# Kernel tuning notes

Hardware: AMD Instinct MI355X
Metric: run time of the kernel (lower is better)

The kernel has to match this reference:

```python
import jax, jax.numpy as jnp
import numpy as np

# --- model dims (from init_kwargs: d_model=2048, num_heads=16, d_conv=4, expand_v=2) ---
D_MODEL = 2048
N_HEADS = 16
D_HEAD = D_MODEL // N_HEADS          # 128
EXPAND_V = 2
KEY_DIM = N_HEADS * D_HEAD           # 2048
VALUE_DIM = KEY_DIM * EXPAND_V       # 4096
HEAD_V = D_HEAD * EXPAND_V           # 256
D_CONV = 4
CONV_CH = 2 * KEY_DIM + VALUE_DIM    # 8192 (q,k,v channels)
TOTAL_PROJ = 2 * KEY_DIM + 2 * VALUE_DIM + 2 * N_HEADS  # 12320
SPLITS = np.cumsum([KEY_DIM, KEY_DIM, VALUE_DIM, VALUE_DIM, N_HEADS]).tolist()


def setup_inputs() -> dict:
    key = jax.random.key(0)
    k0, k1, k2, k3 = jax.random.split(key, 4)
    B, L = 2, 2048
    return {
        "hidden_states": jax.random.normal(k0, (B, L, D_MODEL), jnp.float32),
        "W_qkvgba": jax.random.normal(k1, (D_MODEL, TOTAL_PROJ), jnp.float32) * 0.02,
        "W_conv": jax.random.normal(k2, (CONV_CH, D_CONV), jnp.float32) * 0.1,
        "A_log": jax.random.normal(k3, (N_HEADS,), jnp.float32) * 0.1,
        "dt_bias": jnp.zeros((N_HEADS,), jnp.float32),
    }


def _l2norm(x, eps=1e-6):
    return x * jax.lax.rsqrt(jnp.sum(x * x, axis=-1, keepdims=True) + eps)


def reference(hidden_states, W_qkvgba, W_conv, A_log, dt_bias):
    B, L, _ = hidden_states.shape
    # fused qkv / gate / beta / A projection
    proj = hidden_states @ W_qkvgba                      # [B, L, 12320]
    q, k, v, gate, b, A = jnp.split(proj, SPLITS, axis=-1)

    # depthwise causal short conv over q,k,v channels, then SiLU
    qkv = jnp.concatenate([q, k, v], axis=-1)            # [B, L, CONV_CH]
    x = qkv.transpose(0, 2, 1)                           # [B, C, L]
    kern = W_conv[:, None, :]                            # [C, 1, D_CONV]
    y = jax.lax.conv_general_dilated(
        x, kern, window_strides=(1,), padding=[(D_CONV - 1, 0)],
        feature_group_count=CONV_CH)
    y = jax.nn.silu(y).transpose(0, 2, 1)                # [B, L, C]
    q, k, v = jnp.split(y, [KEY_DIM, 2 * KEY_DIM], axis=-1)

    q = q.reshape(B, L, N_HEADS, D_HEAD)
    k = k.reshape(B, L, N_HEADS, D_HEAD)
    v = v.reshape(B, L, N_HEADS, HEAD_V)

    # L2 norm of q,k (use_qk_l2norm_in_kernel=True)
    q = _l2norm(q)
    k = _l2norm(k)
    scale = D_HEAD ** -0.5

    beta = jax.nn.sigmoid(b)                             # [B, L, H]
    g = -jnp.exp(A_log) * jax.nn.softplus(A + dt_bias)   # [B, L, H] (log decay <= 0)

    # gated delta-rule recurrence over time (scan); state S: [B, H, dk, dv]
    qT = q.transpose(1, 0, 2, 3)
    kT = k.transpose(1, 0, 2, 3)
    vT = v.transpose(1, 0, 2, 3)
    gT = g.transpose(1, 0, 2)
    bT = beta.transpose(1, 0, 2)

    def step(S, inp):
        qt, kt, vt, gt, bt = inp
        S = S * jnp.exp(gt)[..., None, None]
        kv = jnp.einsum('bhk,bhkv->bhv', kt, S)          # current memory readout at k
        delta = (vt - kv) * bt[..., None]                # delta-rule error, gated by beta
        S = S + jnp.einsum('bhk,bhv->bhkv', kt, delta)
        ot = jnp.einsum('bhk,bhkv->bhv', qt * scale, S)
        return S, ot

    S0 = jnp.zeros((B, N_HEADS, D_HEAD, HEAD_V), jnp.float32)
    _, oT = jax.lax.scan(step, S0, (qT, kT, vT, gT, bT))
    o = oT.transpose(1, 0, 2, 3)                         # [B, L, H, HEAD_V]

    # output gating: o * silu(gate)
    gate = gate.reshape(B, L, N_HEADS, HEAD_V)
    return o * jax.nn.silu(gate)
```

## Files before the change

### kernel.cpp

```cpp
#include <hip/hip_runtime.h>
#include <hip/hip_bf16.h>
#include <hip/hip_fp16.h>
#include <math.h>

#define L_SEQ 2048
#define DM    2048
#define NH    16
#define DH    128
#define HVD   256
#define NPROJ 12320
#define QKVW  8192
#define GW    4128

#define NTILE_N 97
#define KSTEPS  64

typedef _Float16 v8h __attribute__((ext_vector_type(8)));
typedef float f32x4 __attribute__((ext_vector_type(4)));
typedef float f32x16 __attribute__((ext_vector_type(16)));

__device__ __forceinline__ void gload_lds16(const void* g, void* l) {
  __builtin_amdgcn_global_load_lds((const __attribute__((address_space(1))) void*)g,
                                   (__attribute__((address_space(3))) void*)l, 16, 0, 0);
}

__device__ __forceinline__ void splitw(float x, unsigned short& h, unsigned short& l) {
  _Float16 hh = (_Float16)x;
  _Float16 ll = (_Float16)(x - (float)hh);
  h = *(unsigned short*)&hh;
  l = *(unsigned short*)&ll;
}
__device__ __forceinline__ float h2f(unsigned short u) {
  return (float)(*(_Float16*)&u);
}

#define MFMA3(acc, ah, al, bh_, bl_)                                          \
  acc = __builtin_amdgcn_mfma_f32_16x16x32_f16(ah, bh_, acc, 0, 0, 0);        \
  acc = __builtin_amdgcn_mfma_f32_16x16x32_f16(ah, bl_, acc, 0, 0, 0);        \
  acc = __builtin_amdgcn_mfma_f32_16x16x32_f16(al, bh_, acc, 0, 0, 0);

#define MFMA3W(acc, ah, al, bh_, bl_)                                         \
  acc = __builtin_amdgcn_mfma_f32_32x32x16_f16(ah, bh_, acc, 0, 0, 0);        \
  acc = __builtin_amdgcn_mfma_f32_32x32x16_f16(ah, bl_, acc, 0, 0, 0);        \
  acc = __builtin_amdgcn_mfma_f32_32x32x16_f16(al, bh_, acc, 0, 0, 0);

__global__ __launch_bounds__(256) void pack_A_k(const float* __restrict__ H, _Float16* __restrict__ Ap) {
  const int mtile = blockIdx.x >> 6, kstep = blockIdx.x & 63;
  const size_t base = (size_t)blockIdx.x * 2 * 4096;
#pragma unroll
  for (int it = 0; it < 2; ++it) {
    int s = threadIdx.x + it * 256;
    int g = s >> 7, r = s & 127;
    const float* src = H + ((size_t)(mtile * 128 + r)) * 2048 + kstep * 32 + g * 8;
    float4 x0 = *(const float4*)src;
    float4 x1 = *(const float4*)(src + 4);
    float xs[8] = {x0.x, x0.y, x0.z, x0.w, x1.x, x1.y, x1.z, x1.w};
    v8h hi, lo;
#pragma unroll
    for (int j = 0; j < 8; ++j) {
      float v = xs[j] * 16.f;
      _Float16 h = (_Float16)v;
      hi[j] = h;
      lo[j] = (_Float16)(v - (float)h);
    }
    *(v8h*)(Ap + base + g * 1024 + r * 8) = hi;
    *(v8h*)(Ap + base + 4096 + g * 1024 + r * 8) = lo;
  }
}

__global__ __launch_bounds__(256) void pack_B_k(const float* __restrict__ W, _Float16* __restrict__ Bp) {
  const int ntile = blockIdx.x >> 6, kstep = blockIdx.x & 63;
  const size_t base = (size_t)blockIdx.x * 2 * 4096;
#pragma unroll
  for (int it = 0; it < 2; ++it) {
    int s = threadIdx.x + it * 256;
    int g = s >> 7, col = s & 127;
    int n = ntile * 128 + col;
    v8h hi, lo;
#pragma unroll
    for (int j = 0; j < 8; ++j) {
      int k = kstep * 32 + g * 8 + j;
      float v = (n < NPROJ) ? W[(size_t)k * NPROJ + n] * 1024.f : 0.f;
      _Float16 h = (_Float16)v;
      hi[j] = h;
      lo[j] = (_Float16)(v - (float)h);
    }
    *(v8h*)(Bp + base + g * 1024 + col * 8) = hi;
    *(v8h*)(Bp + base + 4096 + g * 1024 + col * 8) = lo;
  }
}

__global__ __launch_bounds__(256) void gemm_mfma_k(const _Float16* __restrict__ Ap,
                                                   const _Float16* __restrict__ Bp,
                                                   float* __restrict__ Cq,
                                                   float* __restrict__ Cg) {
  __shared__ _Float16 lds[2][16384];
  const int tid = threadIdx.x;
  const int mtile = blockIdx.x & 31;
  const int ntile = blockIdx.x >> 5;
  const int wid = tid >> 6, lane = tid & 63;
  const int wm = wid >> 1, wn = wid & 1;
  const int lrow = lane & 31, kg = lane >> 5;

  f32x16 acc[2][2];
#pragma unroll
  for (int i = 0; i < 2; ++i)
#pragma unroll
    for (int j = 0; j < 2; ++j)
#pragma unroll
      for (int r = 0; r < 16; ++r) acc[i][j][r] = 0.f;

  const int arow0 = (wm * 64 + lrow) * 8;
  const int bcol0 = (wn * 64 + lrow) * 8;

  const _Float16* Asrc = Ap + ((size_t)(mtile * KSTEPS) * 2) * 4096 + tid * 8;
  const _Float16* Bsrc = Bp + ((size_t)(ntile * KSTEPS) * 2) * 4096 + tid * 8;

#define STAGE(KS, BUF)                                                         \
  {                                                                            \
    const _Float16* An_ = Asrc + (size_t)(KS) * 8192;                          \
    const _Float16* Bn_ = Bsrc + (size_t)(KS) * 8192;                          \
    _Pragma("unroll")                                                          \
    for (int r = 0; r < 4; ++r) {                                              \
      gload_lds16(An_ + r * 2048, &lds[BUF][r * 2048 + tid * 8]);              \
      gload_lds16(Bn_ + r * 2048, &lds[BUF][8192 + r * 2048 + tid * 8]);       \
    }                                                                          \
  }

  STAGE(0, 0);
  STAGE(1, 1);

  for (int kstep = 0; kstep < KSTEPS; ++kstep) {
    const int p = kstep & 1;
    if (kstep + 1 < KSTEPS) {
      asm volatile("s_waitcnt vmcnt(8)" ::: "memory");
    } else {
      asm volatile("s_waitcnt vmcnt(0)" ::: "memory");
    }
    __builtin_amdgcn_sched_barrier(0);
    __builtin_amdgcn_s_barrier();
    __builtin_amdgcn_sched_barrier(0);

#pragma unroll
    for (int ksub = 0; ksub < 2; ++ksub) {
      const int base = (ksub * 2 + kg) * 1024;
      v8h ah0 = *(const v8h*)&lds[p][base + arow0];
      v8h ah1 = *(const v8h*)&lds[p][base + arow0 + 256];
      v8h al0 = *(const v8h*)&lds[p][4096 + base + arow0];
      v8h al1 = *(const v8h*)&lds[p][4096 + base + arow0 + 256];
      v8h bh0 = *(const v8h*)&lds[p][8192 + base + bcol0];
      v8h bh1 = *(const v8h*)&lds[p][8192 + base + bcol0 + 256];
      v8h bl0 = *(const v8h*)&lds[p][12288 + base + bcol0];
      v8h bl1 = *(const v8h*)&lds[p][12288 + base + bcol0 + 256];
      MFMA3W(acc[0][0], ah0, al0, bh0, bl0);
      MFMA3W(acc[0][1], ah0, al0, bh1, bl1);
      MFMA3W(acc[1][0], ah1, al1, bh0, bl0);
      MFMA3W(acc[1][1], ah1, al1, bh1, bl1);
    }
    __builtin_amdgcn_sched_barrier(0);
    __builtin_amdgcn_s_barrier();
    __builtin_amdgcn_sched_barrier(0);
    if (kstep + 2 < KSTEPS) STAGE(kstep + 2, p);
  }
#undef STAGE

  const float sc = 1.f / 16384.f;
#pragma unroll
  for (int tm = 0; tm < 2; ++tm)
#pragma unroll
    for (int tn = 0; tn < 2; ++tn) {
      int col = ntile * 128 + wn * 64 + tn * 32 + lrow;
#pragma unroll
      for (int r = 0; r < 16; ++r) {
        int row = mtile * 128 + wm * 64 + tm * 32 + (r & 3) + 8 * (r >> 2) + 4 * kg;
        float v = acc[tm][tn][r] * sc;
        if (col < QKVW) {
          Cq[(size_t)row * QKVW + col] = v;
        } else if (col < NPROJ) {
          Cg[(size_t)row * GW + (col - QKVW)] = v;
        }
      }
    }
}

__global__ __launch_bounds__(64) void conv_qk_k(
    const float* __restrict__ projQKV, const float* __restrict__ Wc,
    float* __restrict__ qn, float* __restrict__ kn)
{
  const int b = blockIdx.z, hg = blockIdx.y, tc = blockIdx.x;
  const int lane = threadIdx.x;
  const int ch = hg * 128 + lane * 2;
  float4 Wa = *(const float4*)(Wc + (size_t)ch * 4);
  float4 Wb = *(const float4*)(Wc + (size_t)ch * 4 + 4);
  const int t0 = tc * 64;
  const float* P = projQKV + (size_t)b * L_SEQ * QKVW + ch;
  float2 w0 = make_float2(0.f, 0.f), w1 = w0, w2 = w0;
  if (t0 >= 3) w0 = *(const float2*)(P + (size_t)(t0 - 3) * QKVW);
  if (t0 >= 2) w1 = *(const float2*)(P + (size_t)(t0 - 2) * QKVW);
  if (t0 >= 1) w2 = *(const float2*)(P + (size_t)(t0 - 1) * QKVW);
  const bool isq = hg < 16;
  const int h = isq ? hg : hg - 16;
  float* dst = (isq ? qn : kn) + (((size_t)b * NH + h) * L_SEQ) * DH + lane * 2;
  const float sc = isq ? 0.08838834764831845f : 1.f;
  for (int t = t0; t < t0 + 64; ++t) {
    float2 x = *(const float2*)(P + (size_t)t * QKVW);
    float y0 = w0.x * Wa.x + w1.x * Wa.y + w2.x * Wa.z + x.x * Wa.w;
    float y1 = w0.y * Wb.x + w1.y * Wb.y + w2.y * Wb.z + x.y * Wb.w;
    w0 = w1; w1 = w2; w2 = x;
    y0 = y0 / (1.f + expf(-y0));
    y1 = y1 / (1.f + expf(-y1));
    float ss = y0 * y0 + y1 * y1;
#pragma unroll
    for (int off = 1; off < 64; off <<= 1) ss += __shfl_xor(ss, off);
    float nrm = sc / sqrtf(ss + 1e-6f);
    *(float2*)(dst + (size_t)t * DH) = make_float2(y0 * nrm, y1 * nrm);
  }
}

__global__ __launch_bounds__(256) void conv_v_k(
    const float* __restrict__ projQKV, const float* __restrict__ Wc,
    float* __restrict__ vn)
{
  const int b = blockIdx.z, cg = blockIdx.y, tc = blockIdx.x;
  const int vc = (cg * 256 + threadIdx.x) * 4;
  const int ch = 4096 + vc;
  float4 Wv0 = *(const float4*)(Wc + (size_t)ch * 4);
  float4 Wv1 = *(const float4*)(Wc + (size_t)ch * 4 + 4);
  float4 Wv2 = *(const float4*)(Wc + (size_t)ch * 4 + 8);
  float4 Wv3 = *(const float4*)(Wc + (size_t)ch * 4 + 12);
  const int t0 = tc * 64;
  const float* P = projQKV + (size_t)b * L_SEQ * QKVW + ch;
  float4 w0 = make_float4(0.f, 0.f, 0.f, 0.f), w1 = w0, w2 = w0;
  if (t0 >= 3) w0 = *(const float4*)(P + (size_t)(t0 - 3) * QKVW);
  if (t0 >= 2) w1 = *(const float4*)(P + (size_t)(t0 - 2) * QKVW);
  if (t0 >= 1) w2 = *(const float4*)(P + (size_t)(t0 - 1) * QKVW);
  const int h = vc >> 8, vcol = vc & 255;
  float* dst = vn + (((size_t)b * NH + h) * L_SEQ) * HVD + vcol;
  for (int t = t0; t < t0 + 64; ++t) {
    float4 x = *(const float4*)(P + (size_t)t * QKVW);
    float4 y;
    y.x = w0.x * Wv0.x + w1.x * Wv0.y + w2.x * Wv0.z + x.x * Wv0.w;
    y.y = w0.y * Wv1.x + w1.y * Wv1.y + w2.y * Wv1.z + x.y * Wv1.w;
    y.z = w0.z * Wv2.x + w1.z * Wv2.y + w2.z * Wv2.z + x.z * Wv2.w;
    y.w = w0.w * Wv3.x + w1.w * Wv3.y + w2.w * Wv3.z + x.w * Wv3.w;
    w0 = w1; w1 = w2; w2 = x;
    y.x = y.x / (1.f + expf(-y.x));
    y.y = y.y / (1.f + expf(-y.y));
    y.z = y.z / (1.f + expf(-y.z));
    y.w = y.w / (1.f + expf(-y.w));
    *(float4*)(dst + (size_t)t * HVD) = y;
  }
}

__global__ __launch_bounds__(256) void beta_g_k(
    const float* __restrict__ projGate, const float* __restrict__ A_log,
    const float* __restrict__ dt_bias, float* __restrict__ beta, float* __restrict__ g_out)
{
  int idx = blockIdx.x * 256 + threadIdx.x;
  if (idx >= 2 * NH * L_SEQ) return;
  int t = idx & (L_SEQ - 1);
  int h = (idx >> 11) & (NH - 1);
  int b = idx >> 15;
  size_t row = (size_t)(b * L_SEQ + t) * GW;
  float bv = projGate[row + 4096 + h];
  float av = projGate[row + 4112 + h];
  float be = 1.f / (1.f + expf(-bv));
  float xx = av + dt_bias[h];
  float sp = (xx > 20.f) ? xx : log1pf(expf(xx));
  float g = -expf(A_log[h]) * sp;
  beta[idx] = be;
  g_out[idx] = g;
}

__global__ __launch_bounds__(256) void p1_k(
    const float* __restrict__ kn, const float* __restrict__ qn,
    const float* __restrict__ g_arr, const float* __restrict__ beta_arr,
    _Float16* __restrict__ Tg_h, _Float16* __restrict__ Tg_l,
    _Float16* __restrict__ Hg_h, _Float16* __restrict__ Hg_l,
    _Float16* __restrict__ KTg_h, _Float16* __restrict__ KTg_l,
    float* __restrict__ coefG)
{
  __shared__ _Float16 Kh[8192], Kl[8192];
  __shared__ _Float16 QS[16384];
  __shared__ float lc[64], be[64], kw[64];
  _Float16* Qh = QS;
  _Float16* Ql = QS + 8192;
  float* Am = (float*)QS;
  float* Tm = Am + 4096;
  const int cid = blockIdx.x, bh = cid >> 5, ch = cid & 31, t0 = ch * 64;
  const int tid = threadIdx.x, w = tid >> 6, lane = tid & 63, lr = lane & 15, g16 = lane >> 4;

  const float* kb = kn + ((size_t)bh * 2048 + t0) * 128;
  const float* qb = qn + ((size_t)bh * 2048 + t0) * 128;
#pragma unroll
  for (int l = 0; l < 8; ++l) {
    int s = tid + l * 256;
    int row = s >> 5, c = (s & 31) * 4;
    int ad = row * 128 + (c ^ ((row & 7) << 3));
    float4 v = *(const float4*)(kb + (size_t)row * 128 + c);
    ushort4 H, L;
    splitw(v.x * 1024.f, H.x, L.x); splitw(v.y * 1024.f, H.y, L.y);
    splitw(v.z * 1024.f, H.z, L.z); splitw(v.w * 1024.f, H.w, L.w);
    *(ushort4*)&Kh[ad] = H; *(ushort4*)&Kl[ad] = L;
    float4 q = *(const float4*)(qb + (size_t)row * 128 + c);
    splitw(q.x * 1024.f, H.x, L.x); splitw(q.y * 1024.f, H.y, L.y);
    splitw(q.z * 1024.f, H.z, L.z); splitw(q.w * 1024.f, H.w, L.w);
    *(ushort4*)&Qh[ad] = H; *(ushort4*)&Ql[ad] = L;
  }
  if (tid < 64) {
    float x = g_arr[(size_t)bh * 2048 + t0 + tid];
#pragma unroll
    for (int off = 1; off < 64; off <<= 1) { float y = __shfl_up(x, off); if (tid >= off) x += y; }
    lc[tid] = x;
    float x63 = __shfl(x, 63);
    float b_ = beta_arr[(size_t)bh * 2048 + t0 + tid];
    be[tid] = b_;
    kw[tid] = expf(x63 - x);
    float ca = expf(x);
    coefG[(size_t)cid * 192 + tid] = ca;
    coefG[(size_t)cid * 192 + 64 + tid] = b_;
    coefG[(size_t)cid * 192 + 128 + tid] = b_ * ca;
  }
  __syncthreads();
  const float ds20 = 1.f / 1048576.f;
  const int arow = w * 16 + lr, swa = (arow & 7) << 3;
  f32x4 gacc[4];
  for (int nt = 0; nt < 4; ++nt) {
    f32x4 acc = (f32x4){0.f, 0.f, 0.f, 0.f};
    int nrow = nt * 16 + lr, swn = (nrow & 7) << 3;
#pragma unroll
    for (int ks = 0; ks < 4; ++ks) {
      int c = ks * 32 + g16 * 8;
      v8h ah = *(const v8h*)&Kh[arow * 128 + (c ^ swa)];
      v8h al = *(const v8h*)&Kl[arow * 128 + (c ^ swa)];
      v8h bhh = *(const v8h*)&Kh[nrow * 128 + (c ^ swn)];
      v8h bll = *(const v8h*)&Kl[nrow * 128 + (c ^ swn)];
      MFMA3(acc, ah, al, bhh, bll);
    }
    gacc[nt] = acc;
  }
  for (int nt = 0; nt < 4; ++nt) {
    f32x4 acc = (f32x4){0.f, 0.f, 0.f, 0.f};
    int nrow = nt * 16 + lr, swn = (nrow & 7) << 3;
#pragma unroll
    for (int ks = 0; ks < 4; ++ks) {
      int c = ks * 32 + g16 * 8;
      v8h ah = *(const v8h*)&Qh[arow * 128 + (c ^ swa)];
      v8h al = *(const v8h*)&Ql[arow * 128 + (c ^ swa)];
      v8h bhh = *(const v8h*)&Kh[nrow * 128 + (c ^ swn)];
      v8h bll = *(const v8h*)&Kl[nrow * 128 + (c ^ swn)];
      MFMA3(acc, ah, al, bhh, bll);
    }
    int s_ = nt * 16 + lr;
#pragma unroll
    for (int r = 0; r < 4; ++r) {
      int t = w * 16 + g16 * 4 + r;
      float hv = (s_ <= t) ? acc[r] * ds20 * expf(lc[t] - lc[s_]) : 0.f;
      unsigned short hh, ll; splitw(hv * 16384.f, hh, ll);
      size_t go = (size_t)cid * 4096 + t * 64 + (s_ ^ ((t & 7) << 3));
      *(unsigned short*)&Hg_h[go] = hh;
      *(unsigned short*)&Hg_l[go] = ll;
    }
  }
  __syncthreads();
  for (int nt = 0; nt < 4; ++nt) {
    int s_ = nt * 16 + lr;
#pragma unroll
    for (int r = 0; r < 4; ++r) {
      int t = w * 16 + g16 * 4 + r;
      float av = (s_ < t) ? gacc[nt][r] * ds20 * be[t] * expf(lc[t] - lc[s_]) : 0.f;
      Am[t * 64 + s_] = av;
    }
  }
#pragma unroll
  for (int l = 0; l < 16; ++l) { int s2 = tid + l * 256; Tm[s2] = ((s2 >> 6) == (s2 & 63)) ? 1.f : 0.f; }
  for (int s = tid; s < 8192; s += 256) {
    int feat = s >> 6, t = s & 63;
    int ki = t * 128 + (feat ^ ((t & 7) << 3));
    float kvv = ((float)Kh[ki] + (float)Kl[ki]) * kw[t];
    unsigned short hh, ll; splitw(kvv, hh, ll);
    size_t go = (size_t)cid * 8192 + feat * 64 + (t ^ ((feat & 7) << 3));
    *(unsigned short*)&KTg_h[go] = hh;
    *(unsigned short*)&KTg_l[go] = ll;
  }
  __syncthreads();
  if (w == 0) {
    int j = lane;
    for (int t = 1; t < 64; ++t) {
      float sum = 0.f;
      for (int s = 0; s < t; ++s) sum = fmaf(Am[t * 64 + s], Tm[s * 64 + j], sum);
      Tm[t * 64 + j] = ((j == t) ? 1.f : 0.f) - sum;
    }
  }
  __syncthreads();
#pragma unroll
  for (int l = 0; l < 16; ++l) {
    int s2 = tid + l * 256;
    int t = s2 >> 6, sc_ = s2 & 63;
    unsigned short hh, ll; splitw(Tm[s2] * 256.f, hh, ll);
    size_t go = (size_t)cid * 4096 + t * 64 + (sc_ ^ ((t & 7) << 3));
    *(unsigned short*)&Tg_h[go] = hh;
    *(unsigned short*)&Tg_l[go] = ll;
  }
}

__global__ __launch_bounds__(256) void p2_k(
    const float* __restrict__ qn, const float* __restrict__ kn, const float* __restrict__ vn,
    const float* __restrict__ projGate,
    const _Float16* __restrict__ Tg_h, const _Float16* __restrict__ Tg_l,
    const _Float16* __restrict__ Hg_h, const _Float16* __restrict__ Hg_l,
    const _Float16* __restrict__ KTg_h, const _Float16* __restrict__ KTg_l,
    const float* __restrict__ coefG, float* __restrict__ out)
{
  __shared__ _Float16 St_h[4096], St_l[4096];
  __shared__ _Float16 KQ0[8192], KQ1[8192];
  __shared__ _Float16 KTs_h[8192], KTs_l[8192];
  __shared__ _Float16 Ts_h[4096], Ts_l[4096];
  __shared__ _Float16 Hs_h[4096], Hs_l[4096];
  __shared__ float cf[192];

  const int blk = blockIdx.x;
  const int vb = blk >> 5, bh = blk & 31;
  const int b = bh >> 4, h = bh & 15, v0 = vb * 32;
  const int tid = threadIdx.x, w = tid >> 6, lane = tid & 63, lr = lane & 15, g16 = lane >> 4;

  _Float16* BT_h = &KQ0[0];
  _Float16* BT_l = &KQ0[4096];
  _Float16* UT_h = &KQ1[0];
  _Float16* UT_l = &KQ1[4096];

#pragma unroll
  for (int l = 0; l < 8; ++l) { ((unsigned int*)St_h)[tid + l * 256] = 0u; }
#pragma unroll
  for (int l = 0; l < 8; ++l) { ((unsigned int*)St_l)[tid + l * 256] = 0u; }

  const float* qbase = qn + ((size_t)bh * 2048) * 128;
  const float* kbase = kn + ((size_t)bh * 2048) * 128;
  const float* gp = projGate + ((size_t)b * 2048) * GW + h * 256 + v0;
  const float i2_16 = 1.f / 65536.f;
  const float i2_20 = 1.f / 1048576.f;
  const float uscale = 1.f / 256.f;
  const float sscale = 64.f / 65536.f;

  for (int ch = 0; ch < 32; ++ch) {
    const int cid = bh * 32 + ch, t0 = ch * 64;
    {
      const _Float16* th = Tg_h + (size_t)cid * 4096;
      const _Float16* tl = Tg_l + (size_t)cid * 4096;
      const _Float16* hh = Hg_h + (size_t)cid * 4096;
      const _Float16* hl = Hg_l + (size_t)cid * 4096;
      const _Float16* kth = KTg_h + (size_t)cid * 8192;
      const _Float16* ktl = KTg_l + (size_t)cid * 8192;
#pragma unroll
      for (int l = 0; l < 2; ++l) {
        int i = tid + l * 256;
        gload_lds16(th + i * 8, &Ts_h[i * 8]);
        gload_lds16(tl + i * 8, &Ts_l[i * 8]);
        gload_lds16(hh + i * 8, &Hs_h[i * 8]);
        gload_lds16(hl + i * 8, &Hs_l[i * 8]);
      }
#pragma unroll
      for (int l = 0; l < 4; ++l) {
        int i = tid + l * 256;
        gload_lds16(kth + i * 8, &KTs_h[i * 8]);
        gload_lds16(ktl + i * 8, &KTs_l[i * 8]);
      }
      if (tid < 48) gload_lds16(coefG + (size_t)cid * 192 + tid * 4, &cf[tid * 4]);
#pragma unroll
      for (int l = 0; l < 8; ++l) {
        int s = tid + l * 256;
        int row = s >> 5, c = (s & 31) * 4;
        float4 v = *(const float4*)(qbase + (size_t)(t0 + row) * 128 + c);
        ushort4 H, L;
        splitw(v.x * 1024.f, H.x, L.x); splitw(v.y * 1024.f, H.y, L.y);
        splitw(v.z * 1024.f, H.z, L.z); splitw(v.w * 1024.f, H.w, L.w);
        int ad = row * 128 + (c ^ ((row & 7) << 3));
        *(ushort4*)&KQ0[ad] = H; *(ushort4*)&KQ1[ad] = L;
      }
    }
    __syncthreads();
    const float cc = cf[63];
    f32x4 Oacc[2];
    {
      const int arow = w * 16 + lr, swa = (arow & 7) << 3;
      for (int nt = 0; nt < 2; ++nt) {
        f32x4 acc = (f32x4){0.f, 0.f, 0.f, 0.f};
        const int n = nt * 16 + lr, swn = (n & 7) << 3;
#pragma unroll
        for (int ks = 0; ks < 4; ++ks) {
          int c = ks * 32 + g16 * 8;
          v8h ah = *(const v8h*)&KQ0[arow * 128 + (c ^ swa)];
          v8h al = *(const v8h*)&KQ1[arow * 128 + (c ^ swa)];
          v8h bhh = *(const v8h*)&St_h[n * 128 + (c ^ swn)];
          v8h bll = *(const v8h*)&St_l[n * 128 + (c ^ swn)];
          MFMA3(acc, ah, al, bhh, bll);
        }
        Oacc[nt] = acc;
      }
      float4 cav = *(float4*)&cf[w * 16 + g16 * 4];
#pragma unroll
      for (int nt = 0; nt < 2; ++nt) {
        Oacc[nt][0] *= cav.x * 16.f; Oacc[nt][1] *= cav.y * 16.f;
        Oacc[nt][2] *= cav.z * 16.f; Oacc[nt][3] *= cav.w * 16.f;
      }
    }
    __syncthreads();
#pragma unroll
    for (int l = 0; l < 8; ++l) {
      int s = tid + l * 256;
      int row = s >> 5, c = (s & 31) * 4;
      float4 v = *(const float4*)(kbase + (size_t)(t0 + row) * 128 + c);
      ushort4 H, L;
      splitw(v.x * 1024.f, H.x, L.x); splitw(v.y * 1024.f, H.y, L.y);
      splitw(v.z * 1024.f, H.z, L.z); splitw(v.w * 1024.f, H.w, L.w);
      int ad = row * 128 + (c ^ ((row & 7) << 3));
      *(ushort4*)&KQ0[ad] = H; *(ushort4*)&KQ1[ad] = L;
    }
    __syncthreads();
    ushort4 pBh[2], pBl[2];
    {
      const int arow = w * 16 + lr, swa = (arow & 7) << 3;
      float4 cb1v = *(float4*)&cf[64 + w * 16 + g16 * 4];
      float4 cb2v = *(float4*)&cf[128 + w * 16 + g16 * 4];
      for (int nt = 0; nt < 2; ++nt) {
        f32x4 acc = (f32x4){0.f, 0.f, 0.f, 0.f};
        const int n = nt * 16 + lr, swn = (n & 7) << 3;
#pragma unroll
        for (int ks = 0; ks < 4; ++ks) {
          int c = ks * 32 + g16 * 8;
          v8h ah = *(const v8h*)&KQ0[arow * 128 + (c ^ swa)];
          v8h al = *(const v8h*)&KQ1[arow * 128 + (c ^ swa)];
          v8h bhh = *(const v8h*)&St_h[n * 128 + (c ^ swn)];
          v8h bll = *(const v8h*)&St_l[n * 128 + (c ^ swn)];
          MFMA3(acc, ah, al, bhh, bll);
        }
        float cb1a[4] = {cb1v.x, cb1v.y, cb1v.z, cb1v.w};
        float cb2a[4] = {cb2v.x, cb2v.y, cb2v.z, cb2v.w};
        unsigned short* ph = (unsigned short*)&pBh[nt];
        unsigned short* pl = (unsigned short*)&pBl[nt];
#pragma unroll
        for (int r = 0; r < 4; ++r) {
          int t = w * 16 + g16 * 4 + r;
          float kv = acc[r] * i2_16;
          float Vv = vn[((size_t)bh * 2048 + t0 + t) * 256 + v0 + n];
          float Bv = cb1a[r] * Vv - cb2a[r] * kv;
          splitw(Bv * 64.f, ph[r], pl[r]);
        }
      }
    }
    __syncthreads();
    {
      const int tb = w * 16 + g16 * 4;
      for (int nt = 0; nt < 2; ++nt) {
        const int n = nt * 16 + lr, swn = (n & 7) << 3;
        int ad = n * 64 + (tb ^ swn);
        *(ushort4*)&BT_h[ad] = pBh[nt];
        *(ushort4*)&BT_l[ad] = pBl[nt];
      }
    }
    __syncthreads();
    {
      const int arow = w * 16 + lr, swa = (arow & 7) << 3;
      const int tb = w * 16 + g16 * 4;
      for (int nt = 0; nt < 2; ++nt) {
        f32x4 acc = (f32x4){0.f, 0.f, 0.f, 0.f};
        const int n = nt * 16 + lr, swn = (n & 7) << 3;
#pragma unroll
        for (int ks = 0; ks < 2; ++ks) {
          int c = ks * 32 + g16 * 8;
          v8h ah = *(const v8h*)&Ts_h[arow * 64 + (c ^ swa)];
          v8h al = *(const v8h*)&Ts_l[arow * 64 + (c ^ swa)];
          v8h bhh = *(const v8h*)&BT_h[n * 64 + (c ^ swn)];
          v8h bll = *(const v8h*)&BT_l[n * 64 + (c ^ swn)];
          MFMA3(acc, ah, al, bhh, bll);
        }
        ushort4 H, L;
        unsigned short* ph = (unsigned short*)&H;
        unsigned short* pl = (unsigned short*)&L;
#pragma unroll
        for (int r = 0; r < 4; ++r) splitw(acc[r] * uscale, ph[r], pl[r]);
        int ad = n * 64 + (tb ^ swn);
        *(ushort4*)&UT_h[ad] = H;
        *(ushort4*)&UT_l[ad] = L;
      }
    }
    __syncthreads();
    {
      const int arow = w * 16 + lr, swa = (arow & 7) << 3;
      for (int nt = 0; nt < 2; ++nt) {
        const int n = nt * 16 + lr, swn = (n & 7) << 3;
#pragma unroll
        for (int ks = 0; ks < 2; ++ks) {
          int c = ks * 32 + g16 * 8;
          v8h ah = *(const v8h*)&Hs_h[arow * 64 + (c ^ swa)];
          v8h al = *(const v8h*)&Hs_l[arow * 64 + (c ^ swa)];
          v8h bhh = *(const v8h*)&UT_h[n * 64 + (c ^ swn)];
          v8h bll = *(const v8h*)&UT_l[n * 64 + (c ^ swn)];
          MFMA3(Oacc[nt], ah, al, bhh, bll);
        }
      }
      for (int nt = 0; nt < 2; ++nt) {
        const int n = nt * 16 + lr;
#pragma unroll
        for (int r = 0; r < 4; ++r) {
          int t = t0 + w * 16 + g16 * 4 + r;
          float Ov = Oacc[nt][r] * i2_20;
          float gv = gp[(size_t)t * GW + n];
          out[((size_t)b * 2048 + t) * 4096 + h * 256 + v0 + n] = Ov * (gv / (1.f + expf(-gv)));
        }
      }
    }
    {
      const float cc1024 = cc * 1024.f;
#pragma unroll
      for (int m2 = w * 2; m2 < w * 2 + 2; ++m2) {
        const int arow = m2 * 16 + lr, swa = (arow & 7) << 3;
        const int fb = m2 * 16 + g16 * 4;
        for (int nt = 0; nt < 2; ++nt) {
          const int n = nt * 16 + lr, swn = (n & 7) << 3;
          int sad = n * 128 + (fb ^ swn);
          ushort4 sh4 = *(ushort4*)&St_h[sad];
          ushort4 sl4 = *(ushort4*)&St_l[sad];
          f32x4 acc;
          acc[0] = cc1024 * (h2f(sh4.x) + h2f(sl4.x));
          acc[1] = cc1024 * (h2f(sh4.y) + h2f(sl4.y));
          acc[2] = cc1024 * (h2f(sh4.z) + h2f(sl4.z));
          acc[3] = cc1024 * (h2f(sh4.w) + h2f(sl4.w));
#pragma unroll
          for (int ks = 0; ks < 2; ++ks) {
            int c = ks * 32 + g16 * 8;
            v8h ah = *(const v8h*)&KTs_h[arow * 64 + (c ^ swa)];
            v8h al = *(const v8h*)&KTs_l[arow * 64 + (c ^ swa)];
            v8h bhh = *(const v8h*)&UT_h[n * 64 + (c ^ swn)];
            v8h bll = *(const v8h*)&UT_l[n * 64 + (c ^ swn)];
            MFMA3(acc, ah, al, bhh, bll);
          }
          ushort4 H, L;
          unsigned short* ph = (unsigned short*)&H;
          unsigned short* pl = (unsigned short*)&L;
#pragma unroll
          for (int r = 0; r < 4; ++r) splitw(acc[r] * sscale, ph[r], pl[r]);
          *(ushort4*)&St_h[sad] = H;
          *(ushort4*)&St_l[sad] = L;
        }
      }
    }
    __syncthreads();
  }
}

extern "C" void kernel_launch(void* const* d_in, const int* in_sizes, int n_in,
                              void* d_out, int out_size, void* d_ws, size_t ws_size,
                              hipStream_t stream) {
  const float* hidden  = (const float*)d_in[0];
  const float* W       = (const float*)d_in[1];
  const float* Wc      = (const float*)d_in[2];
  const float* A_log   = (const float*)d_in[3];
  const float* dt_bias = (const float*)d_in[4];
  float* out = (float*)d_out;

  char* ws = (char*)d_ws;
  _Float16* Ap = (_Float16*)ws;
  _Float16* Bp = (_Float16*)(ws + (size_t)33554432);
  float* qn    = (float*)ws;
  float* kn    = qn + (size_t)8388608;
  float* vn    = kn + (size_t)8388608;
  float* g_arr = vn + (size_t)16777216;
  float* beta  = g_arr + (size_t)65536;
  float* projQKV = (float*)(ws + (size_t)135266304);
  char*  tb0 = ws + (size_t)135266304;
  _Float16* Tg_h  = (_Float16*)tb0;
  _Float16* Tg_l  = (_Float16*)(tb0 + (size_t)8388608);
  _Float16* Hg_h  = (_Float16*)(tb0 + (size_t)16777216);
  _Float16* Hg_l  = (_Float16*)(tb0 + (size_t)25165824);
  _Float16* KTg_h = (_Float16*)(tb0 + (size_t)33554432);
  _Float16* KTg_l = (_Float16*)(tb0 + (size_t)50331648);
  float*    coefG = (float*)   (tb0 + (size_t)67108864);
  float* projGate = (float*)(ws + (size_t)269484032);

  pack_A_k<<<32 * KSTEPS, 256, 0, stream>>>(hidden, Ap);
  pack_B_k<<<NTILE_N * KSTEPS, 256, 0, stream>>>(W, Bp);
  gemm_mfma_k<<<32 * NTILE_N, 256, 0, stream>>>(Ap, Bp, projQKV, projGate);

  conv_qk_k<<<dim3(32, 32, 2), 64, 0, stream>>>(projQKV, Wc, qn, kn);
  conv_v_k<<<dim3(32, 4, 2), 256, 0, stream>>>(projQKV, Wc, vn);
  beta_g_k<<<(2 * NH * L_SEQ + 255) / 256, 256, 0, stream>>>(projGate, A_log, dt_bias, beta, g_arr);

  p1_k<<<1024, 256, 0, stream>>>(kn, qn, g_arr, beta, Tg_h, Tg_l, Hg_h, Hg_l, KTg_h, KTg_l, coefG);
  p2_k<<<256, 256, 0, stream>>>(qn, kn, vn, projGate, Tg_h, Tg_l, Hg_h, Hg_l, KTg_h, KTg_l, coefG, out);
}
```

Measured before the change: 1.091 ms.

## Pre-split q/k to swizzled fp16 hi/lo in conv, stream into LDS directly

```diff
diff --git a/kernel.cpp b/kernel.cpp
--- a/kernel.cpp
+++ b/kernel.cpp
@@ -17,7 +17,6 @@
 
 typedef _Float16 v8h __attribute__((ext_vector_type(8)));
 typedef float f32x4 __attribute__((ext_vector_type(4)));
-typedef float f32x16 __attribute__((ext_vector_type(16)));
 
 __device__ __forceinline__ void gload_lds16(const void* g, void* l) {
   __builtin_amdgcn_global_load_lds((const __attribute__((address_space(1))) void*)g,
@@ -38,11 +37,6 @@
   acc = __builtin_amdgcn_mfma_f32_16x16x32_f16(ah, bh_, acc, 0, 0, 0);        \
   acc = __builtin_amdgcn_mfma_f32_16x16x32_f16(ah, bl_, acc, 0, 0, 0);        \
   acc = __builtin_amdgcn_mfma_f32_16x16x32_f16(al, bh_, acc, 0, 0, 0);
-
-#define MFMA3W(acc, ah, al, bh_, bl_)                                         \
-  acc = __builtin_amdgcn_mfma_f32_32x32x16_f16(ah, bh_, acc, 0, 0, 0);        \
-  acc = __builtin_amdgcn_mfma_f32_32x32x16_f16(ah, bl_, acc, 0, 0, 0);        \
-  acc = __builtin_amdgcn_mfma_f32_32x32x16_f16(al, bh_, acc, 0, 0, 0);
 
 __global__ __launch_bounds__(256) void pack_A_k(const float* __restrict__ H, _Float16* __restrict__ Ap) {
   const int mtile = blockIdx.x >> 6, kstep = blockIdx.x & 63;
@@ -100,18 +94,16 @@
   const int ntile = blockIdx.x >> 5;
   const int wid = tid >> 6, lane = tid & 63;
   const int wm = wid >> 1, wn = wid & 1;
-  const int lrow = lane & 31, kg = lane >> 5;
-
-  f32x16 acc[2][2];
-#pragma unroll
-  for (int i = 0; i < 2; ++i)
-#pragma unroll
-    for (int j = 0; j < 2; ++j)
-#pragma unroll
-      for (int r = 0; r < 16; ++r) acc[i][j][r] = 0.f;
-
-  const int arow0 = (wm * 64 + lrow) * 8;
-  const int bcol0 = (wn * 64 + lrow) * 8;
+  const int lrow = lane & 15, g = lane >> 4;
+
+  f32x4 acc[4][4];
+#pragma unroll
+  for (int i = 0; i < 4; ++i)
+#pragma unroll
+    for (int j = 0; j < 4; ++j) acc[i][j] = (f32x4){0.f, 0.f, 0.f, 0.f};
+
+  const int aoff = (wm * 64 + lrow) * 8 + g * 1024;
+  const int boff = (wn * 64 + lrow) * 8 + g * 1024;
 
   const _Float16* Asrc = Ap + ((size_t)(mtile * KSTEPS) * 2) * 4096 + tid * 8;
   const _Float16* Bsrc = Bp + ((size_t)(ntile * KSTEPS) * 2) * 4096 + tid * 8;
@@ -141,22 +133,22 @@
     __builtin_amdgcn_s_barrier();
     __builtin_amdgcn_sched_barrier(0);
 
-#pragma unroll
-    for (int ksub = 0; ksub < 2; ++ksub) {
-      const int base = (ksub * 2 + kg) * 1024;
-      v8h ah0 = *(const v8h*)&lds[p][base + arow0];
-      v8h ah1 = *(const v8h*)&lds[p][base + arow0 + 256];
-      v8h al0 = *(const v8h*)&lds[p][4096 + base + arow0];
-      v8h al1 = *(const v8h*)&lds[p][4096 + base + arow0 + 256];
-      v8h bh0 = *(const v8h*)&lds[p][8192 + base + bcol0];
-      v8h bh1 = *(const v8h*)&lds[p][8192 + base + bcol0 + 256];
-      v8h bl0 = *(const v8h*)&lds[p][12288 + base + bcol0];
-      v8h bl1 = *(const v8h*)&lds[p][12288 + base + bcol0 + 256];
-      MFMA3W(acc[0][0], ah0, al0, bh0, bl0);
-      MFMA3W(acc[0][1], ah0, al0, bh1, bl1);
-      MFMA3W(acc[1][0], ah1, al1, bh0, bl0);
-      MFMA3W(acc[1][1], ah1, al1, bh1, bl1);
-    }
+    v8h ah[4], al[4], bh[4], bl[4];
+#pragma unroll
+    for (int f = 0; f < 4; ++f) {
+      ah[f] = *(const v8h*)&lds[p][aoff + f * 128];
+      al[f] = *(const v8h*)&lds[p][4096 + aoff + f * 128];
+      bh[f] = *(const v8h*)&lds[p][8192 + boff + f * 128];
+      bl[f] = *(const v8h*)&lds[p][12288 + boff + f * 128];
+    }
+#pragma unroll
+    for (int fm = 0; fm < 4; ++fm)
+#pragma unroll
+      for (int fn = 0; fn < 4; ++fn) {
+        acc[fm][fn] = __builtin_amdgcn_mfma_f32_16x16x32_f16(ah[fm], bh[fn], acc[fm][fn], 0, 0, 0);
+        acc[fm][fn] = __builtin_amdgcn_mfma_f32_16x16x32_f16(ah[fm], bl[fn], acc[fm][fn], 0, 0, 0);
+        acc[fm][fn] = __builtin_amdgcn_mfma_f32_16x16x32_f16(al[fm], bh[fn], acc[fm][fn], 0, 0, 0);
+      }
     __builtin_amdgcn_sched_barrier(0);
     __builtin_amdgcn_s_barrier();
     __builtin_amdgcn_sched_barrier(0);
@@ -166,26 +158,29 @@
 
   const float sc = 1.f / 16384.f;
 #pragma unroll
-  for (int tm = 0; tm < 2; ++tm)
-#pragma unroll
-    for (int tn = 0; tn < 2; ++tn) {
-      int col = ntile * 128 + wn * 64 + tn * 32 + lrow;
-#pragma unroll
-      for (int r = 0; r < 16; ++r) {
-        int row = mtile * 128 + wm * 64 + tm * 32 + (r & 3) + 8 * (r >> 2) + 4 * kg;
-        float v = acc[tm][tn][r] * sc;
-        if (col < QKVW) {
-          Cq[(size_t)row * QKVW + col] = v;
-        } else if (col < NPROJ) {
-          Cg[(size_t)row * GW + (col - QKVW)] = v;
-        }
-      }
-    }
+  for (int fm = 0; fm < 4; ++fm) {
+    int row = mtile * 128 + wm * 64 + fm * 16 + g * 4;
+#pragma unroll
+    for (int fn = 0; fn < 4; ++fn) {
+      int col = ntile * 128 + wn * 64 + fn * 16 + lrow;
+      if (col < QKVW) {
+#pragma unroll
+        for (int r = 0; r < 4; ++r)
+          Cq[(size_t)(row + r) * QKVW + col] = acc[fm][fn][r] * sc;
+      } else if (col < NPROJ) {
+        int lcol = col - QKVW;
+#pragma unroll
+        for (int r = 0; r < 4; ++r)
+          Cg[(size_t)(row + r) * GW + lcol] = acc[fm][fn][r] * sc;
+      }
+    }
+  }
 }
 
 __global__ __launch_bounds__(64) void conv_qk_k(
     const float* __restrict__ projQKV, const float* __restrict__ Wc,
-    float* __restrict__ qn, float* __restrict__ kn)
+    _Float16* __restrict__ qh, _Float16* __restrict__ ql,
+    _Float16* __restrict__ kh, _Float16* __restrict__ kl)
 {
   const int b = blockIdx.z, hg = blockIdx.y, tc = blockIdx.x;
   const int lane = threadIdx.x;
@@ -200,8 +195,9 @@
   if (t0 >= 1) w2 = *(const float2*)(P + (size_t)(t0 - 1) * QKVW);
   const bool isq = hg < 16;
   const int h = isq ? hg : hg - 16;
-  float* dst = (isq ? qn : kn) + (((size_t)b * NH + h) * L_SEQ) * DH + lane * 2;
-  const float sc = isq ? 0.08838834764831845f : 1.f;
+  _Float16* dh = (isq ? qh : kh) + (((size_t)b * NH + h) * L_SEQ) * 128;
+  _Float16* dl = (isq ? ql : kl) + (((size_t)b * NH + h) * L_SEQ) * 128;
+  const float sc = (isq ? 0.08838834764831845f : 1.f) * 1024.f;
   for (int t = t0; t < t0 + 64; ++t) {
     float2 x = *(const float2*)(P + (size_t)t * QKVW);
     float y0 = w0.x * Wa.x + w1.x * Wa.y + w2.x * Wa.z + x.x * Wa.w;
@@ -213,7 +209,12 @@
 #pragma unroll
     for (int off = 1; off < 64; off <<= 1) ss += __shfl_xor(ss, off);
     float nrm = sc / sqrtf(ss + 1e-6f);
-    *(float2*)(dst + (size_t)t * DH) = make_float2(y0 * nrm, y1 * nrm);
+    unsigned short h0, l0, h1, l1;
+    splitw(y0 * nrm, h0, l0);
+    splitw(y1 * nrm, h1, l1);
+    int idx = t * 128 + ((lane * 2) ^ ((t & 7) << 3));
+    *(unsigned int*)&dh[idx] = (unsigned int)h0 | ((unsigned int)h1 << 16);
+    *(unsigned int*)&dl[idx] = (unsigned int)l0 | ((unsigned int)l1 << 16);
   }
 }
 
@@ -273,7 +274,8 @@
 }
 
 __global__ __launch_bounds__(256) void p1_k(
-    const float* __restrict__ kn, const float* __restrict__ qn,
+    const _Float16* __restrict__ kh_g, const _Float16* __restrict__ kl_g,
+    const _Float16* __restrict__ qh_g, const _Float16* __restrict__ ql_g,
     const float* __restrict__ g_arr, const float* __restrict__ beta_arr,
     _Float16* __restrict__ Tg_h, _Float16* __restrict__ Tg_l,
     _Float16* __restrict__ Hg_h, _Float16* __restrict__ Hg_l,
@@ -290,22 +292,14 @@
   const int cid = blockIdx.x, bh = cid >> 5, ch = cid & 31, t0 = ch * 64;
   const int tid = threadIdx.x, w = tid >> 6, lane = tid & 63, lr = lane & 15, g16 = lane >> 4;
 
-  const float* kb = kn + ((size_t)bh * 2048 + t0) * 128;
-  const float* qb = qn + ((size_t)bh * 2048 + t0) * 128;
-#pragma unroll
-  for (int l = 0; l < 8; ++l) {
-    int s = tid + l * 256;
-    int row = s >> 5, c = (s & 31) * 4;
-    int ad = row * 128 + (c ^ ((row & 7) << 3));
-    float4 v = *(const float4*)(kb + (size_t)row * 128 + c);
-    ushort4 H, L;
-    splitw(v.x * 1024.f, H.x, L.x); splitw(v.y * 1024.f, H.y, L.y);
-    splitw(v.z * 1024.f, H.z, L.z); splitw(v.w * 1024.f, H.w, L.w);
-    *(ushort4*)&Kh[ad] = H; *(ushort4*)&Kl[ad] = L;
-    float4 q = *(const float4*)(qb + (size_t)row * 128 + c);
-    splitw(q.x * 1024.f, H.x, L.x); splitw(q.y * 1024.f, H.y, L.y);
-    splitw(q.z * 1024.f, H.z, L.z); splitw(q.w * 1024.f, H.w, L.w);
-    *(ushort4*)&Qh[ad] = H; *(ushort4*)&Ql[ad] = L;
+  const size_t gb = ((size_t)bh * 2048 + t0) * 128;
+#pragma unroll
+  for (int l = 0; l < 4; ++l) {
+    int i = (tid + l * 256) * 8;
+    gload_lds16(kh_g + gb + i, &Kh[i]);
+    gload_lds16(kl_g + gb + i, &Kl[i]);
+    gload_lds16(qh_g + gb + i, &Qh[i]);
+    gload_lds16(ql_g + gb + i, &Ql[i]);
   }
   if (tid < 64) {
     float x = g_arr[(size_t)bh * 2048 + t0 + tid];
@@ -405,8 +399,9 @@
 }
 
 __global__ __launch_bounds__(256) void p2_k(
-    const float* __restrict__ qn, const float* __restrict__ kn, const float* __restrict__ vn,
-    const float* __restrict__ projGate,
+    const _Float16* __restrict__ qh_g, const _Float16* __restrict__ ql_g,
+    const _Float16* __restrict__ kh_g, const _Float16* __restrict__ kl_g,
+    const float* __restrict__ vn, const float* __restrict__ projGate,
     const _Float16* __restrict__ Tg_h, const _Float16* __restrict__ Tg_l,
     const _Float16* __restrict__ Hg_h, const _Float16* __restrict__ Hg_l,
     const _Float16* __restrict__ KTg_h, const _Float16* __restrict__ KTg_l,
@@ -414,6 +409,7 @@
 {
   __shared__ _Float16 St_h[4096], St_l[4096];
   __shared__ _Float16 KQ0[8192], KQ1[8192];
+  __shared__ _Float16 KK0[8192], KK1[8192];
   __shared__ _Float16 KTs_h[8192], KTs_l[8192];
   __shared__ _Float16 Ts_h[4096], Ts_l[4096];
   __shared__ _Float16 Hs_h[4096], Hs_l[4096];
@@ -434,8 +430,6 @@
 #pragma unroll
   for (int l = 0; l < 8; ++l) { ((unsigned int*)St_l)[tid + l * 256] = 0u; }
 
-  const float* qbase = qn + ((size_t)bh * 2048) * 128;
-  const float* kbase = kn + ((size_t)bh * 2048) * 128;
   const float* gp = projGate + ((size_t)b * 2048) * GW + h * 256 + v0;
   const float i2_16 = 1.f / 65536.f;
   const float i2_20 = 1.f / 1048576.f;
@@ -451,38 +445,38 @@
       const _Float16* hl = Hg_l + (size_t)cid * 4096;
       const _Float16* kth = KTg_h + (size_t)cid * 8192;
       const _Float16* ktl = KTg_l + (size_t)cid * 8192;
+      const size_t gb = ((size_t)bh * 2048 + t0) * 128;
 #pragma unroll
       for (int l = 0; l < 2; ++l) {
-        int i = tid + l * 256;
-        gload_lds16(th + i * 8, &Ts_h[i * 8]);
-        gload_lds16(tl + i * 8, &Ts_l[i * 8]);
-        gload_lds16(hh + i * 8, &Hs_h[i * 8]);
-        gload_lds16(hl + i * 8, &Hs_l[i * 8]);
+        int i = (tid + l * 256) * 8;
+        gload_lds16(th + i, &Ts_h[i]);
+        gload_lds16(tl + i, &Ts_l[i]);
+        gload_lds16(hh + i, &Hs_h[i]);
+        gload_lds16(hl + i, &Hs_l[i]);
       }
 #pragma unroll
       for (int l = 0; l < 4; ++l) {
-        int i = tid + l * 256;
-        gload_lds16(kth + i * 8, &KTs_h[i * 8]);
-        gload_lds16(ktl + i * 8, &KTs_l[i * 8]);
+        int i = (tid + l * 256) * 8;
+        gload_lds16(kth + i, &KTs_h[i]);
+        gload_lds16(ktl + i, &KTs_l[i]);
+        gload_lds16(qh_g + gb + i, &KQ0[i]);
+        gload_lds16(ql_g + gb + i, &KQ1[i]);
+        gload_lds16(kh_g + gb + i, &KK0[i]);
+        gload_lds16(kl_g + gb + i, &KK1[i]);
       }
       if (tid < 48) gload_lds16(coefG + (size_t)cid * 192 + tid * 4, &cf[tid * 4]);
-#pragma unroll
-      for (int l = 0; l < 8; ++l) {
-        int s = tid + l * 256;
-        int row = s >> 5, c = (s & 31) * 4;
-        float4 v = *(const float4*)(qbase + (size_t)(t0 + row) * 128 + c);
-        ushort4 H, L;
-        splitw(v.x * 1024.f, H.x, L.x); splitw(v.y * 1024.f, H.y, L.y);
-        splitw(v.z * 1024.f, H.z, L.z); splitw(v.w * 1024.f, H.w, L.w);
-        int ad = row * 128 + (c ^ ((row & 7) << 3));
-        *(ushort4*)&KQ0[ad] = H; *(ushort4*)&KQ1[ad] = L;
-      }
-    }
+    }
+    float Vv[2][4];
+#pragma unroll
+    for (int nt = 0; nt < 2; ++nt)
+#pragma unroll
+      for (int r = 0; r < 4; ++r)
+        Vv[nt][r] = vn[((size_t)bh * 2048 + t0 + w * 16 + g16 * 4 + r) * 256 + v0 + nt * 16 + lr];
     __syncthreads();
     const float cc = cf[63];
+    const int arow = w * 16 + lr, swa = (arow & 7) << 3;
     f32x4 Oacc[2];
     {
-      const int arow = w * 16 + lr, swa = (arow & 7) << 3;
       for (int nt = 0; nt < 2; ++nt) {
         f32x4 acc = (f32x4){0.f, 0.f, 0.f, 0.f};
         const int n = nt * 16 + lr, swn = (n & 7) << 3;
@@ -504,22 +498,8 @@
         Oacc[nt][2] *= cav.z * 16.f; Oacc[nt][3] *= cav.w * 16.f;
       }
     }
-    __syncthreads();
-#pragma unroll
-    for (int l = 0; l < 8; ++l) {
-      int s = tid + l * 256;
-      int row = s >> 5, c = (s & 31) * 4;
-      float4 v = *(const float4*)(kbase + (size_t)(t0 + row) * 128 + c);
-      ushort4 H, L;
-      splitw(v.x * 1024.f, H.x, L.x); splitw(v.y * 1024.f, H.y, L.y);
-      splitw(v.z * 1024.f, H.z, L.z); splitw(v.w * 1024.f, H.w, L.w);
-      int ad = row * 128 + (c ^ ((row & 7) << 3));
-      *(ushort4*)&KQ0[ad] = H; *(ushort4*)&KQ1[ad] = L;
-    }
-    __syncthreads();
     ushort4 pBh[2], pBl[2];
     {
-      const int arow = w * 16 + lr, swa = (arow & 7) << 3;
       float4 cb1v = *(float4*)&cf[64 + w * 16 + g16 * 4];
       float4 cb2v = *(float4*)&cf[128 + w * 16 + g16 * 4];
       for (int nt = 0; nt < 2; ++nt) {
@@ -528,8 +508,8 @@
 #pragma unroll
         for (int ks = 0; ks < 4; ++ks) {
           int c = ks * 32 + g16 * 8;
-          v8h ah = *(const v8h*)&KQ0[arow * 128 + (c ^ swa)];
-          v8h al = *(const v8h*)&KQ1[arow * 128 + (c ^ swa)];
+          v8h ah = *(const v8h*)&KK0[arow * 128 + (c ^ swa)];
+          v8h al = *(const v8h*)&KK1[arow * 128 + (c ^ swa)];
           v8h bhh = *(const v8h*)&St_h[n * 128 + (c ^ swn)];
           v8h bll = *(const v8h*)&St_l[n * 128 + (c ^ swn)];
           MFMA3(acc, ah, al, bhh, bll);
@@ -540,10 +520,8 @@
         unsigned short* pl = (unsigned short*)&pBl[nt];
 #pragma unroll
         for (int r = 0; r < 4; ++r) {
-          int t = w * 16 + g16 * 4 + r;
           float kv = acc[r] * i2_16;
-          float Vv = vn[((size_t)bh * 2048 + t0 + t) * 256 + v0 + n];
-          float Bv = cb1a[r] * Vv - cb2a[r] * kv;
+          float Bv = cb1a[r] * Vv[nt][r] - cb2a[r] * kv;
           splitw(Bv * 64.f, ph[r], pl[r]);
         }
       }
@@ -560,7 +538,6 @@
     }
     __syncthreads();
     {
-      const int arow = w * 16 + lr, swa = (arow & 7) << 3;
       const int tb = w * 16 + g16 * 4;
       for (int nt = 0; nt < 2; ++nt) {
         f32x4 acc = (f32x4){0.f, 0.f, 0.f, 0.f};
@@ -586,7 +563,6 @@
     }
     __syncthreads();
     {
-      const int arow = w * 16 + lr, swa = (arow & 7) << 3;
       for (int nt = 0; nt < 2; ++nt) {
         const int n = nt * 16 + lr, swn = (n & 7) << 3;
 #pragma unroll
@@ -609,12 +585,10 @@
           out[((size_t)b * 2048 + t) * 4096 + h * 256 + v0 + n] = Ov * (gv / (1.f + expf(-gv)));
         }
       }
-    }
-    {
       const float cc1024 = cc * 1024.f;
 #pragma unroll
       for (int m2 = w * 2; m2 < w * 2 + 2; ++m2) {
-        const int arow = m2 * 16 + lr, swa = (arow & 7) << 3;
+        const int ar2 = m2 * 16 + lr, swa2 = (ar2 & 7) << 3;
         const int fb = m2 * 16 + g16 * 4;
         for (int nt = 0; nt < 2; ++nt) {
           const int n = nt * 16 + lr, swn = (n & 7) << 3;
@@ -629,8 +603,8 @@
 #pragma unroll
           for (int ks = 0; ks < 2; ++ks) {
             int c = ks * 32 + g16 * 8;
-            v8h ah = *(const v8h*)&KTs_h[arow * 64 + (c ^ swa)];
-            v8h al = *(const v8h*)&KTs_l[arow * 64 + (c ^ swa)];
+            v8h ah = *(const v8h*)&KTs_h[ar2 * 64 + (c ^ swa2)];
+            v8h al = *(const v8h*)&KTs_l[ar2 * 64 + (c ^ swa2)];
             v8h bhh = *(const v8h*)&UT_h[n * 64 + (c ^ swn)];
             v8h bll = *(const v8h*)&UT_l[n * 64 + (c ^ swn)];
             MFMA3(acc, ah, al, bhh, bll);
@@ -662,11 +636,13 @@
   char* ws = (char*)d_ws;
   _Float16* Ap = (_Float16*)ws;
   _Float16* Bp = (_Float16*)(ws + (size_t)33554432);
-  float* qn    = (float*)ws;
-  float* kn    = qn + (size_t)8388608;
-  float* vn    = kn + (size_t)8388608;
-  float* g_arr = vn + (size_t)16777216;
-  float* beta  = g_arr + (size_t)65536;
+  _Float16* qh = (_Float16*)ws;
+  _Float16* ql = (_Float16*)(ws + (size_t)16777216);
+  _Float16* kh = (_Float16*)(ws + (size_t)33554432);
+  _Float16* kl = (_Float16*)(ws + (size_t)50331648);
+  float* vn    = (float*)(ws + (size_t)67108864);
+  float* g_arr = (float*)(ws + (size_t)134217728);
+  float* beta  = (float*)(ws + (size_t)134479872);
   float* projQKV = (float*)(ws + (size_t)135266304);
   char*  tb0 = ws + (size_t)135266304;
   _Float16* Tg_h  = (_Float16*)tb0;
@@ -682,10 +658,10 @@
   pack_B_k<<<NTILE_N * KSTEPS, 256, 0, stream>>>(W, Bp);
   gemm_mfma_k<<<32 * NTILE_N, 256, 0, stream>>>(Ap, Bp, projQKV, projGate);
 
-  conv_qk_k<<<dim3(32, 32, 2), 64, 0, stream>>>(projQKV, Wc, qn, kn);
+  conv_qk_k<<<dim3(32, 32, 2), 64, 0, stream>>>(projQKV, Wc, qh, ql, kh, kl);
   conv_v_k<<<dim3(32, 4, 2), 256, 0, stream>>>(projQKV, Wc, vn);
   beta_g_k<<<(2 * NH * L_SEQ + 255) / 256, 256, 0, stream>>>(projGate, A_log, dt_bias, beta, g_arr);
 
-  p1_k<<<1024, 256, 0, stream>>>(kn, qn, g_arr, beta, Tg_h, Tg_l, Hg_h, Hg_l, KTg_h, KTg_l, coefG);
-  p2_k<<<256, 256, 0, stream>>>(qn, kn, vn, projGate, Tg_h, Tg_l, Hg_h, Hg_l, KTg_h, KTg_l, coefG, out);
-}
+  p1_k<<<1024, 256, 0, stream>>>(kh, kl, qh, ql, g_arr, beta, Tg_h, Tg_l, Hg_h, Hg_l, KTg_h, KTg_l, coefG);
+  p2_k<<<256, 256, 0, stream>>>(qh, ql, kh, kl, vn, projGate, Tg_h, Tg_l, Hg_h, Hg_l, KTg_h, KTg_l, coefG, out);
+}
```

Result: faster. 1.022 ms (-6.3%).
